# Kernel tuning notes

Measured on AMD Instinct MI355X. Metric: run time of the kernel, lower is better.

## Reference

```python
import jax, jax.numpy as jnp
import numpy as np

CLUSTER_DIM = 64
SHRINKAGE = True
EPS = 1e-8


def setup_inputs() -> dict:
    key = jax.random.key(0)
    x = jax.random.normal(key, (256, CLUSTER_DIM, 4096), dtype=jnp.float32)
    return {"x": x}


def _mat_shrinkage(C, n):
    # Rao-Blackwellized Ledoit-Wolf shrinkage toward scaled identity.
    p = CLUSTER_DIM
    I = jnp.eye(p, dtype=C.dtype)[None, :, :]
    trace = jnp.trace(C, axis1=-2, axis2=-1)[:, None, None]          # [B,1,1]
    F_hat = trace / p * I
    second_trace = jnp.einsum('bij,bji->b', C, C)[:, None, None]      # tr(C @ C)
    numerator = (n - 2) / n * second_trace + trace ** 2
    denominator = (n + 2) * (second_trace - trace ** 2 / p)
    rho = jnp.minimum(numerator / denominator, 1.0)
    return rho * F_hat + (1.0 - rho) * C


def reference(x):
    B, C, M = x.shape  # C == CLUSTER_DIM
    x_mu = jnp.mean(x, axis=2, keepdims=True)
    x_cnt = x - x_mu                                                  # [B,C,M]
    cov = jnp.einsum('bcm,bdm->bcd', x_cnt, x_cnt) / M                # [B,C,C]
    if SHRINKAGE:
        cov = _mat_shrinkage(cov, n=M)
    L, Q = jnp.linalg.eigh(cov)                                       # L:[B,C] Q:[B,C,C]
    L = jnp.maximum(L, EPS)
    # S_hat = Q @ diag(L^-1/2) @ Q^T, fused as scaled columns of Q
    S_hat = jnp.einsum('bik,bk,bjk->bij', Q, jax.lax.rsqrt(L), Q)     # [B,C,C]
    Z = jnp.einsum('bij,bjm->bim', S_hat, x_cnt)                      # [B,C,M]
    return Z
```

## Files before the change

kernel.cpp:

```cpp
#include <hip/hip_runtime.h>
#include <hip/hip_bf16.h>

#define BB 256
#define P 64
#define MM 4096
#define MC 128
#define MT 256

using bf16x8 = __attribute__((ext_vector_type(8))) short;
using f32x16 = __attribute__((ext_vector_type(16))) float;

__device__ inline f32x16 MF(bf16x8 a, bf16x8 b, f32x16 c) {
    return __builtin_amdgcn_mfma_f32_32x32x16_bf16(a, b, c, 0, 0, 0);
}
__device__ inline unsigned cvtpk(float lo, float hi) {
    unsigned u;
    asm("v_cvt_pk_bf16_f32 %0, %1, %2" : "=v"(u) : "v"(lo), "v"(hi));
    return u;
}

__global__ __launch_bounds__(256)
void covpart_kernel(const float* __restrict__ x, float* __restrict__ s2p,
                    float* __restrict__ s1p, int nsplit)
{
    __shared__ __align__(16) unsigned char smem[17408];
    char* xh = (char*)smem;

    const int b = blockIdx.x, sp = blockIdx.y;
    const int t = threadIdx.x;
    const int w = t >> 6, l = t & 63;
    const int lr = l & 31, lh = l >> 5;
    const int mlen = MM / nsplit;
    const float* xb = x + (size_t)b * (P * MM) + (size_t)sp * mlen;

    f32x16 acc0 = {0,0,0,0,0,0,0,0,0,0,0,0,0,0,0,0};
    f32x16 acc1 = {0,0,0,0,0,0,0,0,0,0,0,0,0,0,0,0};
    f32x16 acc2 = {0,0,0,0,0,0,0,0,0,0,0,0,0,0,0,0};
    float s1a[8] = {0.f,0.f,0.f,0.f,0.f,0.f,0.f,0.f};

    const int kbase = lh * 16;

    const int nch = mlen / MC;
    for (int ch = 0; ch < nch; ++ch) {
        const int m0 = ch * MC;
        __syncthreads();
        float4 v[8];
        #pragma unroll
        for (int j = 0; j < 8; ++j) {
            int f4 = t + 256 * j;
            int r = f4 >> 5, c = (f4 & 31) << 2;
            v[j] = *reinterpret_cast<const float4*>(xb + (size_t)r * MM + m0 + c);
        }
        #pragma unroll
        for (int j = 0; j < 8; ++j) {
            int f4 = t + 256 * j;
            int r = f4 >> 5, c4 = f4 & 31;
            float e0 = v[j].x, e1 = v[j].y, e2 = v[j].z, e3 = v[j].w;
            s1a[j] += (e0 + e1) + (e2 + e3);
            uint2 hp;
            hp.x = cvtpk(e0, e1);
            hp.y = cvtpk(e2, e3);
            *reinterpret_cast<uint2*>(xh + r * 272 + c4 * 8) = hp;
        }
        __syncthreads();
        #pragma unroll
        for (int kk = 0; kk < 2; ++kk) {
            const int kb = (2 * w + kk) * 32 + kbase;
            bf16x8 f0 = *(const bf16x8*)(xh + lr * 272 + kb);
            bf16x8 f1 = *(const bf16x8*)(xh + (32 + lr) * 272 + kb);
            acc0 = MF(f0, f0, acc0);
            acc1 = MF(f0, f1, acc1);
            acc2 = MF(f1, f1, acc2);
        }
    }

    float (*T)[32][33] = reinterpret_cast<float (*)[32][33]>(smem);
    float* s2b = s2p + ((size_t)sp * BB + b) * (P * P);

#define REDUCE_PASS(ACC, STORE)                                       \
    {                                                                 \
        __syncthreads();                                              \
        _Pragma("unroll")                                             \
        for (int n = 0; n < 16; ++n) {                                \
            int row = (n & 3) + 8 * (n >> 2) + 4 * lh;                \
            T[w][row][lr] = ACC[n];                                   \
        }                                                             \
        __syncthreads();                                              \
        _Pragma("unroll")                                             \
        for (int q = 0; q < 4; ++q) {                                 \
            int idx = t + 256 * q;                                    \
            int r = idx >> 5, c = idx & 31;                           \
            float s = T[0][r][c] + T[1][r][c] + T[2][r][c] + T[3][r][c]; \
            STORE                                                     \
        }                                                             \
    }

    REDUCE_PASS(acc0, s2b[r * 64 + c] = s;)
    REDUCE_PASS(acc1, s2b[r * 64 + 32 + c] = s; s2b[(32 + c) * 64 + r] = s;)
    REDUCE_PASS(acc2, s2b[(32 + r) * 64 + 32 + c] = s;)
#undef REDUCE_PASS

    #pragma unroll
    for (int m = 16; m >= 1; m >>= 1) {
        #pragma unroll
        for (int j = 0; j < 8; ++j) s1a[j] += __shfl_xor(s1a[j], m);
    }
    if ((l & 31) == 0) {
        float* s1b = s1p + ((size_t)sp * BB + b) * P;
        int r0 = 2 * w + lh;
        #pragma unroll
        for (int j = 0; j < 8; ++j) s1b[r0 + 8 * j] = s1a[j];
    }
}

typedef float (*Mat68)[68];

__device__ inline void mm64f(Mat68 D, Mat68 A, Mat68 Bm, int t, float alpha, float beta)
{
    __syncthreads();
    const int r0 = (t >> 4) * 4, c0 = (t & 15) * 4;
    float acc[4][4];
    #pragma unroll
    for (int i = 0; i < 4; ++i)
        #pragma unroll
        for (int j = 0; j < 4; ++j) acc[i][j] = 0.f;
    #pragma unroll 4
    for (int k = 0; k < P; ++k) {
        float av[4], bv[4];
        *reinterpret_cast<float4*>(av) = *reinterpret_cast<const float4*>(&A[k][r0]);
        *reinterpret_cast<float4*>(bv) = *reinterpret_cast<const float4*>(&Bm[k][c0]);
        #pragma unroll
        for (int i = 0; i < 4; ++i)
            #pragma unroll
            for (int j = 0; j < 4; ++j) acc[i][j] += av[i] * bv[j];
    }
    __syncthreads();
    #pragma unroll
    for (int i = 0; i < 4; ++i)
        #pragma unroll
        for (int j = 0; j < 4; ++j)
            D[r0 + i][c0 + j] = alpha * acc[i][j] + ((r0 + i) == (c0 + j) ? beta : 0.f);
}

__global__ __launch_bounds__(256)
void whiten_kernel(const float* __restrict__ s2p, const float* __restrict__ s1p,
                   unsigned* __restrict__ sbb, float* __restrict__ tvec, int nsplit)
{
    __shared__ __align__(16) float B0[P][68], B1[P][68], B2[P][68], B3[P][68], B4[P][68];
    __shared__ float mus[P];
    __shared__ float red[2][4];
    const int b = blockIdx.x, t = threadIdx.x;

    if (t < P) {
        float s = 0.f;
        for (int sp = 0; sp < nsplit; ++sp) s += s1p[((size_t)sp * BB + b) * P + t];
        mus[t] = s * (1.0f / MM);
    }
    __syncthreads();

    float tr_part = 0.f, s2_part = 0.f;
    #pragma unroll
    for (int j = 0; j < 16; ++j) {
        int f = t + 256 * j;
        int i = f >> 6, jc = f & 63;
        float sum = 0.f;
        for (int sp = 0; sp < nsplit; ++sp)
            sum += s2p[((size_t)sp * BB + b) * (P * P) + f];
        float v = sum * (1.0f / MM) - mus[i] * mus[jc];
        B0[i][jc] = v;
        s2_part += v * v;
        if (i == jc) tr_part += v;
    }
    #pragma unroll
    for (int off = 32; off > 0; off >>= 1) {
        tr_part += __shfl_down(tr_part, off);
        s2_part += __shfl_down(s2_part, off);
    }
    if ((t & 63) == 0) { red[0][t >> 6] = tr_part; red[1][t >> 6] = s2_part; }
    __syncthreads();
    const float trace = red[0][0] + red[0][1] + red[0][2] + red[0][3];
    const float sum2  = red[1][0] + red[1][1] + red[1][2] + red[1][3];

    const float nf = (float)MM;
    const float num = (nf - 2.0f) / nf * sum2 + trace * trace;
    const float den = (nf + 2.0f) * (sum2 - trace * trace / (float)P);
    const float rho = (den > 0.f) ? fminf(num / den, 1.0f) : 1.0f;
    const float lam = trace * (1.0f / P);
    const float inv_s = 1.0f / lam;

    #pragma unroll
    for (int j = 0; j < 16; ++j) {
        int f = t + 256 * j;
        int i = f >> 6, jc = f & 63;
        float v = B0[i][jc];
        float sv = ((1.0f - rho) * v + ((i == jc) ? rho * lam : 0.f)) * inv_s;
        B0[i][jc] = sv;
        B2[i][jc] = ((i == jc) ? 1.5f : 0.f) - 0.5f * sv;
    }

    mm64f(B1, B0, B2, t, 1.f, 0.f);
    Mat68 Yc = B1, Zc = B2, Tc = B0, U = B3, V = B4;
    {
        mm64f(Tc, Zc, Yc, t, -0.5f, 1.5f);
        mm64f(U,  Yc, Tc, t, 1.f, 0.f);
        mm64f(V,  Tc, Zc, t, 1.f, 0.f);
        Mat68 tmp = Yc; Yc = U; U = tmp;
        tmp = Zc; Zc = V; V = tmp;
    }
    mm64f(Tc, Zc, Yc, t, -0.5f, 1.5f);
    mm64f(U,  Tc, Zc, t, 1.f, 0.f);
    __syncthreads();

    const float sc = rsqrtf(lam);
    unsigned* sb = sbb + (size_t)b * (P * P / 2);
    #pragma unroll
    for (int j = 0; j < 8; ++j) {
        int f2 = t + 256 * j;
        int i = f2 >> 5, jc = (f2 & 31) * 2;
        sb[f2] = cvtpk(U[i][jc] * sc, U[i][jc + 1] * sc);
    }
    if (t < P) {
        float tv = 0.f;
        #pragma unroll
        for (int d = 0; d < P; ++d) tv += U[t][d] * mus[d];
        tvec[b * P + t] = tv * sc;
    }
}

__global__ __launch_bounds__(256)
void apply_kernel(const float* __restrict__ x, const unsigned* __restrict__ sbb,
                  const float* __restrict__ tvec, float* __restrict__ out)
{
    __shared__ __align__(16) unsigned short Sb[P][72];
    __shared__ __align__(16) unsigned Xpk[32][260];
    __shared__ float tvs[P];
    const int mt = blockIdx.x, b = blockIdx.y;
    const int t = threadIdx.x;
    const int w = t >> 6, l = t & 63;
    const int lr = l & 31, lh = l >> 5;

    const unsigned* sb = sbb + (size_t)b * (P * P / 2);
    #pragma unroll
    for (int j = 0; j < 8; ++j) {
        int slot = t + 256 * j;
        int row = slot >> 5, cu = slot & 31;
        *reinterpret_cast<unsigned*>(&Sb[row][cu * 2]) = sb[slot];
    }
    if (t < P) tvs[t] = tvec[b * P + t];

    const float* xb = x + (size_t)b * (P * MM) + mt * MT;
    #pragma unroll
    for (int j = 0; j < 8; ++j) {
        int slot = t + 256 * j;
        int dp = slot >> 6, m0 = (slot & 63) * 4;
        const float* xr = xb + (size_t)(2 * dp) * MM + m0;
        float4 a = *reinterpret_cast<const float4*>(xr);
        float4 c = *reinterpret_cast<const float4*>(xr + MM);
        unsigned u0 = cvtpk(a.x, c.x), u1 = cvtpk(a.y, c.y);
        unsigned u2 = cvtpk(a.z, c.z), u3 = cvtpk(a.w, c.w);
        uint4 pk = make_uint4(u0, u1, u2, u3);
        *reinterpret_cast<uint4*>(&Xpk[dp][m0]) = pk;
    }
    __syncthreads();

    f32x16 acc00 = {0,0,0,0,0,0,0,0,0,0,0,0,0,0,0,0};
    f32x16 acc01 = {0,0,0,0,0,0,0,0,0,0,0,0,0,0,0,0};
    f32x16 acc10 = {0,0,0,0,0,0,0,0,0,0,0,0,0,0,0,0};
    f32x16 acc11 = {0,0,0,0,0,0,0,0,0,0,0,0,0,0,0,0};

    const int cq0 = (2 * w) * 32 + lr, cq1 = (2 * w + 1) * 32 + lr;
    #pragma unroll
    for (int ks = 0; ks < 4; ++ks) {
        const char* arow = (const char*)&Sb[0][0] + ks * 32 + lh * 16;
        bf16x8 a0 = *(const bf16x8*)(arow + lr * 144);
        bf16x8 a1 = *(const bf16x8*)(arow + (32 + lr) * 144);
        const int dpb = ks * 8 + lh * 4;
        union { unsigned u[4]; bf16x8 v; } b0, b1;
        #pragma unroll
        for (int q = 0; q < 4; ++q) {
            b0.u[q] = Xpk[dpb + q][cq0];
            b1.u[q] = Xpk[dpb + q][cq1];
        }
        acc00 = MF(a0, b0.v, acc00);
        acc01 = MF(a0, b1.v, acc01);
        acc10 = MF(a1, b0.v, acc10);
        acc11 = MF(a1, b1.v, acc11);
    }

    float* ob = out + (size_t)b * (P * MM) + mt * MT;
#define STORE_TILE(ACC, RT, CQ)                                          \
    {                                                                    \
        _Pragma("unroll")                                                \
        for (int n = 0; n < 16; ++n) {                                   \
            int row = (RT) * 32 + (n & 3) + 8 * (n >> 2) + 4 * lh;       \
            ob[(size_t)row * MM + (CQ)] = ACC[n] - tvs[row];             \
        }                                                                \
    }
    STORE_TILE(acc00, 0, cq0)
    STORE_TILE(acc01, 0, cq1)
    STORE_TILE(acc10, 1, cq0)
    STORE_TILE(acc11, 1, cq1)
#undef STORE_TILE
}

extern "C" void kernel_launch(void* const* d_in, const int* in_sizes, int n_in,
                              void* d_out, int out_size, void* d_ws, size_t ws_size,
                              hipStream_t stream)
{
    const float* x = (const float*)d_in[0];
    float* out = (float*)d_out;

    auto need = [](int ns) -> size_t {
        return ((size_t)ns * BB * P * P + (size_t)ns * BB * P
                + (size_t)BB * P * P / 2 + (size_t)BB * P) * sizeof(float);
    };
    int nsplit = 4;
    if (ws_size < need(4)) nsplit = 2;
    if (ws_size < need(2)) nsplit = 1;

    float* s2p  = (float*)d_ws;
    float* s1p  = s2p + (size_t)nsplit * BB * P * P;
    unsigned* sbb = (unsigned*)(s1p + (size_t)nsplit * BB * P);
    float* tvec = (float*)(sbb + (size_t)BB * P * P / 2);

    covpart_kernel<<<dim3(BB, nsplit), 256, 0, stream>>>(x, s2p, s1p, nsplit);
    whiten_kernel<<<dim3(BB), 256, 0, stream>>>(s2p, s1p, sbb, tvec, nsplit);
    apply_kernel<<<dim3(MM / MT, BB), 256, 0, stream>>>(x, sbb, tvec, out);
}
```

Before: 196.2 us.

## Double-buffer covariance loads and shrink apply tile with packed S layout

The covariance partial kernel now double-buffers its shared-memory bf16 tile and prefetches the next chunk's global loads into registers before the barrier, so memory latency can overlap with MFMA work. The apply kernel halves its column tile (more blocks, fewer accumulators per wave). It also switches the whitening matrix storage to a row-pair packed layout matching the B-operand format, which requires a matching change to how the whiten kernel writes it. The costs are doubled LDS in the covariance kernel and re-reading S for each smaller tile.

Result: no change. 199.7 us (+1.8%).

```diff
diff --git a/kernel.cpp b/kernel.cpp
--- a/kernel.cpp
+++ b/kernel.cpp
@@ -5,7 +5,7 @@
 #define P 64
 #define MM 4096
 #define MC 128
-#define MT 256
+#define MTA 128
 
 using bf16x8 = __attribute__((ext_vector_type(8))) short;
 using f32x16 = __attribute__((ext_vector_type(16))) float;
@@ -23,8 +23,7 @@
 void covpart_kernel(const float* __restrict__ x, float* __restrict__ s2p,
                     float* __restrict__ s1p, int nsplit)
 {
-    __shared__ __align__(16) unsigned char smem[17408];
-    char* xh = (char*)smem;
+    __shared__ __align__(16) unsigned char smem[34816];
 
     const int b = blockIdx.x, sp = blockIdx.y;
     const int t = threadIdx.x;
@@ -39,18 +38,18 @@
     float s1a[8] = {0.f,0.f,0.f,0.f,0.f,0.f,0.f,0.f};
 
     const int kbase = lh * 16;
-
     const int nch = mlen / MC;
+
+    float4 v[8];
+    #pragma unroll
+    for (int j = 0; j < 8; ++j) {
+        int f4 = t + 256 * j;
+        int r = f4 >> 5, c = (f4 & 31) << 2;
+        v[j] = *reinterpret_cast<const float4*>(xb + (size_t)r * MM + c);
+    }
+
     for (int ch = 0; ch < nch; ++ch) {
-        const int m0 = ch * MC;
-        __syncthreads();
-        float4 v[8];
-        #pragma unroll
-        for (int j = 0; j < 8; ++j) {
-            int f4 = t + 256 * j;
-            int r = f4 >> 5, c = (f4 & 31) << 2;
-            v[j] = *reinterpret_cast<const float4*>(xb + (size_t)r * MM + m0 + c);
-        }
+        char* buf = (char*)smem + (ch & 1) * 17408;
         #pragma unroll
         for (int j = 0; j < 8; ++j) {
             int f4 = t + 256 * j;
@@ -60,14 +59,23 @@
             uint2 hp;
             hp.x = cvtpk(e0, e1);
             hp.y = cvtpk(e2, e3);
-            *reinterpret_cast<uint2*>(xh + r * 272 + c4 * 8) = hp;
+            *reinterpret_cast<uint2*>(buf + r * 272 + c4 * 8) = hp;
+        }
+        if (ch + 1 < nch) {
+            const int m0 = (ch + 1) * MC;
+            #pragma unroll
+            for (int j = 0; j < 8; ++j) {
+                int f4 = t + 256 * j;
+                int r = f4 >> 5, c = (f4 & 31) << 2;
+                v[j] = *reinterpret_cast<const float4*>(xb + (size_t)r * MM + m0 + c);
+            }
         }
         __syncthreads();
         #pragma unroll
         for (int kk = 0; kk < 2; ++kk) {
             const int kb = (2 * w + kk) * 32 + kbase;
-            bf16x8 f0 = *(const bf16x8*)(xh + lr * 272 + kb);
-            bf16x8 f1 = *(const bf16x8*)(xh + (32 + lr) * 272 + kb);
+            bf16x8 f0 = *(const bf16x8*)(buf + lr * 272 + kb);
+            bf16x8 f1 = *(const bf16x8*)(buf + (32 + lr) * 272 + kb);
             acc0 = MF(f0, f0, acc0);
             acc1 = MF(f0, f1, acc1);
             acc2 = MF(f1, f1, acc2);
@@ -215,9 +223,9 @@
     unsigned* sb = sbb + (size_t)b * (P * P / 2);
     #pragma unroll
     for (int j = 0; j < 8; ++j) {
-        int f2 = t + 256 * j;
-        int i = f2 >> 5, jc = (f2 & 31) * 2;
-        sb[f2] = cvtpk(U[i][jc] * sc, U[i][jc + 1] * sc);
+        int slot = t + 256 * j;
+        int dp = slot >> 6, row = slot & 63;
+        sb[slot] = cvtpk(U[row][2 * dp] * sc, U[row][2 * dp + 1] * sc);
     }
     if (t < P) {
         float tv = 0.f;
@@ -231,8 +239,8 @@
 void apply_kernel(const float* __restrict__ x, const unsigned* __restrict__ sbb,
                   const float* __restrict__ tvec, float* __restrict__ out)
 {
-    __shared__ __align__(16) unsigned short Sb[P][72];
-    __shared__ __align__(16) unsigned Xpk[32][260];
+    __shared__ unsigned Spk[32][68];
+    __shared__ unsigned Xpk[32][132];
     __shared__ float tvs[P];
     const int mt = blockIdx.x, b = blockIdx.y;
     const int t = threadIdx.x;
@@ -243,64 +251,48 @@
     #pragma unroll
     for (int j = 0; j < 8; ++j) {
         int slot = t + 256 * j;
-        int row = slot >> 5, cu = slot & 31;
-        *reinterpret_cast<unsigned*>(&Sb[row][cu * 2]) = sb[slot];
+        Spk[slot >> 6][slot & 63] = sb[slot];
     }
     if (t < P) tvs[t] = tvec[b * P + t];
 
-    const float* xb = x + (size_t)b * (P * MM) + mt * MT;
-    #pragma unroll
-    for (int j = 0; j < 8; ++j) {
+    const float* xb = x + (size_t)b * (P * MM) + mt * MTA;
+    #pragma unroll
+    for (int j = 0; j < 4; ++j) {
         int slot = t + 256 * j;
-        int dp = slot >> 6, m0 = (slot & 63) * 4;
+        int dp = slot >> 5, m0 = (slot & 31) * 4;
         const float* xr = xb + (size_t)(2 * dp) * MM + m0;
         float4 a = *reinterpret_cast<const float4*>(xr);
         float4 c = *reinterpret_cast<const float4*>(xr + MM);
-        unsigned u0 = cvtpk(a.x, c.x), u1 = cvtpk(a.y, c.y);
-        unsigned u2 = cvtpk(a.z, c.z), u3 = cvtpk(a.w, c.w);
-        uint4 pk = make_uint4(u0, u1, u2, u3);
+        uint4 pk = make_uint4(cvtpk(a.x, c.x), cvtpk(a.y, c.y),
+                              cvtpk(a.z, c.z), cvtpk(a.w, c.w));
         *reinterpret_cast<uint4*>(&Xpk[dp][m0]) = pk;
     }
     __syncthreads();
 
-    f32x16 acc00 = {0,0,0,0,0,0,0,0,0,0,0,0,0,0,0,0};
-    f32x16 acc01 = {0,0,0,0,0,0,0,0,0,0,0,0,0,0,0,0};
-    f32x16 acc10 = {0,0,0,0,0,0,0,0,0,0,0,0,0,0,0,0};
-    f32x16 acc11 = {0,0,0,0,0,0,0,0,0,0,0,0,0,0,0,0};
-
-    const int cq0 = (2 * w) * 32 + lr, cq1 = (2 * w + 1) * 32 + lr;
+    f32x16 acc0 = {0,0,0,0,0,0,0,0,0,0,0,0,0,0,0,0};
+    f32x16 acc1 = {0,0,0,0,0,0,0,0,0,0,0,0,0,0,0,0};
+    const int cq = w * 32 + lr;
     #pragma unroll
     for (int ks = 0; ks < 4; ++ks) {
-        const char* arow = (const char*)&Sb[0][0] + ks * 32 + lh * 16;
-        bf16x8 a0 = *(const bf16x8*)(arow + lr * 144);
-        bf16x8 a1 = *(const bf16x8*)(arow + (32 + lr) * 144);
         const int dpb = ks * 8 + lh * 4;
-        union { unsigned u[4]; bf16x8 v; } b0, b1;
+        union { unsigned u[4]; bf16x8 v; } a0, a1, bb;
         #pragma unroll
         for (int q = 0; q < 4; ++q) {
-            b0.u[q] = Xpk[dpb + q][cq0];
-            b1.u[q] = Xpk[dpb + q][cq1];
+            a0.u[q] = Spk[dpb + q][lr];
+            a1.u[q] = Spk[dpb + q][32 + lr];
+            bb.u[q] = Xpk[dpb + q][cq];
         }
-        acc00 = MF(a0, b0.v, acc00);
-        acc01 = MF(a0, b1.v, acc01);
-        acc10 = MF(a1, b0.v, acc10);
-        acc11 = MF(a1, b1.v, acc11);
-    }
-
-    float* ob = out + (size_t)b * (P * MM) + mt * MT;
-#define STORE_TILE(ACC, RT, CQ)                                          \
-    {                                                                    \
-        _Pragma("unroll")                                                \
-        for (int n = 0; n < 16; ++n) {                                   \
-            int row = (RT) * 32 + (n & 3) + 8 * (n >> 2) + 4 * lh;       \
-            ob[(size_t)row * MM + (CQ)] = ACC[n] - tvs[row];             \
-        }                                                                \
-    }
-    STORE_TILE(acc00, 0, cq0)
-    STORE_TILE(acc01, 0, cq1)
-    STORE_TILE(acc10, 1, cq0)
-    STORE_TILE(acc11, 1, cq1)
-#undef STORE_TILE
+        acc0 = MF(a0.v, bb.v, acc0);
+        acc1 = MF(a1.v, bb.v, acc1);
+    }
+
+    float* ob = out + (size_t)b * (P * MM) + mt * MTA;
+    #pragma unroll
+    for (int n = 0; n < 16; ++n) {
+        int r0 = (n & 3) + 8 * (n >> 2) + 4 * lh;
+        ob[(size_t)r0 * MM + cq]        = acc0[n] - tvs[r0];
+        ob[(size_t)(32 + r0) * MM + cq] = acc1[n] - tvs[32 + r0];
+    }
 }
 
 extern "C" void kernel_launch(void* const* d_in, const int* in_sizes, int n_in,
@@ -325,5 +317,5 @@
 
     covpart_kernel<<<dim3(BB, nsplit), 256, 0, stream>>>(x, s2p, s1p, nsplit);
     whiten_kernel<<<dim3(BB), 256, 0, stream>>>(s2p, s1p, sbb, tvec, nsplit);
-    apply_kernel<<<dim3(MM / MT, BB), 256, 0, stream>>>(x, sbb, tvec, out);
-}
+    apply_kernel<<<dim3(MM / MTA, BB), 256, 0, stream>>>(x, sbb, tvec, out);
+}
```
